# Performance work log

Measured on AMD Instinct MI355X. Metric: run time of the kernel, lower is better.

Reference implementation:

```python
import jax, jax.numpy as jnp
import numpy as np

T, A, E, N, W, HID, FD = 4096, 1024, 512, 32768, 10, 150, 20
GI = 2 * A + E  # 2560
BINS = jnp.array([1, 2, 3, 4, 8, 16, 32, 64], dtype=jnp.int32)


def _mlp(x, W1, b1, W2, b2, W3, b3):
    # Score module: Linear->ReLU->Linear->ReLU->Linear->1 (dropout is a no-op in eval)
    h = jax.nn.relu(x @ W1 + b1)
    h = jax.nn.relu(h @ W2 + b2)
    return h @ W3 + b3


def setup_inputs() -> dict:
    key = jax.random.key(0)
    ks = jax.random.split(key, 20)
    s = 0.02
    inp = {
        "states": jax.random.normal(ks[0], (T, A), jnp.float32),
        "embeds": jax.random.normal(ks[1], (T, E), jnp.float32),
        "span_starts": jax.random.randint(ks[2], (N,), 0, T - W, jnp.int32),
        "span_widths": jax.random.randint(ks[3], (N,), 1, W + 1, jnp.int32),
        # attention Score params (input A)
        "Wa1": jax.random.normal(ks[4], (A, HID)) * s, "ba1": jnp.zeros((HID,)),
        "Wa2": jax.random.normal(ks[5], (HID, HID)) * s, "ba2": jnp.zeros((HID,)),
        "Wa3": jax.random.normal(ks[6], (HID, 1)) * s, "ba3": jnp.zeros((1,)),
        # width Feature embedding table: len(bins)+1 = 9 rows
        "width_emb": jax.random.normal(ks[7], (9, FD)) * s,
        # mention Score params (input GI + FD)
        "Ws1": jax.random.normal(ks[8], (GI + FD, HID)) * s, "bs1": jnp.zeros((HID,)),
        "Ws2": jax.random.normal(ks[9], (HID, HID)) * s, "bs2": jnp.zeros((HID,)),
        "Ws3": jax.random.normal(ks[10], (HID, 1)) * s, "bs3": jnp.zeros((1,)),
    }
    return inp


def reference(states, embeds, span_starts, span_widths,
              Wa1, ba1, Wa2, ba2, Wa3, ba3, width_emb,
              Ws1, bs1, Ws2, bs2, Ws3, bs3):
    # per-token attention logits  [T]
    attns = _mlp(states, Wa1, ba1, Wa2, ba2, Wa3, ba3).squeeze(-1)
    offs = jnp.arange(W)                                   # [W]
    pos = span_starts[:, None] + offs[None, :]             # [N, W]
    mask = offs[None, :] < span_widths[:, None]            # ragged span mask
    pos_c = jnp.clip(pos, 0, T - 1)
    logit = jnp.where(mask, attns[pos_c], -jnp.inf)        # [N, W]
    w = jax.nn.softmax(logit, axis=1)                      # per-span softmax
    attn_sum = jnp.einsum('nw,nwe->ne', w, embeds[pos_c])  # [N, E]
    ends = span_starts + span_widths - 1
    bin_idx = jnp.sum(span_widths[:, None] >= BINS[None, :], axis=1)
    size = width_emb[bin_idx]                              # [N, FD]
    g = jnp.concatenate([states[span_starts], states[ends], attn_sum, size], axis=1)
    scores = _mlp(g, Ws1, bs1, Ws2, bs2, Ws3, bs3).squeeze(-1)  # [N]
    return scores
```

## Files before the change

### kernel.cpp

```cpp
#include <hip/hip_runtime.h>
#include <math.h>

#define T_TOK 4096
#define A_DIM 1024
#define E_DIM 512
#define N_SPAN 32768
#define W_MAX 10
#define HID 150
#define FD 20

#define PR  160
#define KP2 160

#define WS_ATTNS 0
#define WS_PB    4096
#define WS_WPACK 1314816
#define WS_SB    1627856
#define WS_EB    3725008
#define PB_P0 0
#define PB_P1 655360
#define PB_P2 1310720
#define PB_P3 1966080
#define WP_ST  0
#define WP_V   491520
#define WP_A2  573440
#define WP_S2  599040
#define WP_WE1 624640
#define WP_TOTAL 626080
#define SB_PIECES 524288
#define EB_PIECES 262144
#define PK_ITEMS (WP_TOTAL + SB_PIECES + EB_PIECES)

typedef short  bf16x8 __attribute__((ext_vector_type(8)));
typedef float  f32x4  __attribute__((ext_vector_type(4)));

__device__ __forceinline__ float4 ld4(const float* p) { return *(const float4*)p; }

__device__ __forceinline__ unsigned short f2bf(float f) {
    unsigned u = __float_as_uint(f);
    unsigned r = u + 0x7fffu + ((u >> 16) & 1u);
    return (unsigned short)(r >> 16);
}
__device__ __forceinline__ float bf2f(short s) {
    return __uint_as_float(((unsigned)(unsigned short)s) << 16);
}
__device__ __forceinline__ bf16x8 cvt_frag(const float* p) {
    float4 u = ld4(p), v = ld4(p + 4);
    bf16x8 f;
    f[0] = (short)f2bf(u.x); f[1] = (short)f2bf(u.y);
    f[2] = (short)f2bf(u.z); f[3] = (short)f2bf(u.w);
    f[4] = (short)f2bf(v.x); f[5] = (short)f2bf(v.y);
    f[6] = (short)f2bf(v.z); f[7] = (short)f2bf(v.w);
    return f;
}

__global__ __launch_bounds__(256) void prepack_kernel(
    const float* __restrict__ states, const float* __restrict__ embeds,
    const float* __restrict__ Wa1, const float* __restrict__ Ws1,
    const float* __restrict__ Wa2, const float* __restrict__ Ws2,
    const float* __restrict__ width_emb,
    unsigned short* __restrict__ wp, unsigned short* __restrict__ Sb,
    unsigned short* __restrict__ Eb)
{
    int idx = blockIdx.x * 256 + threadIdx.x;
    if (idx >= PK_ITEMS) return;
    if (idx < WP_TOTAL) {
        float v = 0.f;
        if (idx < WP_V) {
            int gidx = idx / 163840, r = idx % 163840;
            int ngrp = r / 81920, r2 = r % 81920;
            int c = r2 / 2560, d = r2 % 2560;
            int n = d >> 5, qsw = (d >> 3) & 3, off = d & 7;
            int q = qsw ^ ((n >> 1) & 3);
            int k = c * 32 + q * 8 + off;
            int gn = ngrp * 80 + n;
            const float* W = (gidx == 0) ? Wa1 : Ws1 + (size_t)(gidx - 1) * 1024 * HID;
            if (gn < HID) v = W[(size_t)k * HID + gn];
        } else if (idx < WP_A2) {
            int r = idx - WP_V;
            int ngrp = r / 40960, r2 = r % 40960;
            int c = r2 / 2560, d = r2 % 2560;
            int n = d >> 5, qsw = (d >> 3) & 3, off = d & 7;
            int q = qsw ^ ((n >> 1) & 3);
            int k = c * 32 + q * 8 + off;
            int gn = ngrp * 80 + n;
            if (gn < HID) v = Ws1[(size_t)(2048 + k) * HID + gn];
        } else if (idx < WP_S2) {
            int e = idx - WP_A2;
            int n = e / KP2, k = e % KP2;
            if (n < HID && k < HID) v = Wa2[(size_t)k * HID + n];
        } else if (idx < WP_WE1) {
            int e = idx - WP_S2;
            int n = e / KP2, k = e % KP2;
            if (n < HID && k < HID) v = Ws2[(size_t)k * HID + n];
        } else {
            int e = idx - WP_WE1;
            int b = e / KP2, n = e % KP2;
            if (n < HID)
                for (int k = 0; k < FD; ++k)
                    v = fmaf(width_emb[b * FD + k], Ws1[(size_t)(2560 + k) * HID + n], v);
        }
        wp[idx] = f2bf(v);
    } else if (idx < WP_TOTAL + SB_PIECES) {
        int p = idx - WP_TOTAL;
        int mb = p >> 11, r = p & 2047;
        int c = r >> 6, d8 = r & 63;
        int m = d8 >> 2, qsw = d8 & 3;
        int q = qsw ^ ((m >> 1) & 3);
        const float* src = states + (size_t)(mb * 16 + m) * A_DIM + c * 32 + q * 8;
        *(bf16x8*)(Sb + (size_t)p * 8) = cvt_frag(src);
    } else {
        int p = idx - WP_TOTAL - SB_PIECES;
        int mb = p >> 10, r = p & 1023;
        int c = r >> 6, d8 = r & 63;
        int m = d8 >> 2, qsw = d8 & 3;
        int q = qsw ^ ((m >> 1) & 3);
        const float* src = embeds + (size_t)(mb * 16 + m) * E_DIM + c * 32 + q * 8;
        *(bf16x8*)(Eb + (size_t)p * 8) = cvt_frag(src);
    }
}

template<int NCH>
__device__ __forceinline__ void gemm_reg(
    const unsigned short* __restrict__ pA0, const unsigned short* __restrict__ pA1,
    const unsigned short* __restrict__ pB, f32x4 (&acc)[2][5])
{
    bf16x8 a0[2], a1[2], bb[2][5];
#define LDC(c, s) { \
        a0[s] = *(const bf16x8*)(pA0 + (size_t)(c) * 512); \
        a1[s] = *(const bf16x8*)(pA1 + (size_t)(c) * 512); \
        _Pragma("unroll") \
        for (int t = 0; t < 5; ++t) \
            bb[s][t] = *(const bf16x8*)(pB + (size_t)(c) * 2560 + t * 512); }
    LDC(0, 0);
#pragma unroll
    for (int c = 0; c < NCH; ++c) {
        const int s = c & 1;
        if (c + 1 < NCH) LDC(c + 1, s ^ 1);
#pragma unroll
        for (int t = 0; t < 5; ++t) {
            acc[0][t] = __builtin_amdgcn_mfma_f32_16x16x32_bf16(a0[s], bb[s][t], acc[0][t], 0, 0, 0);
            acc[1][t] = __builtin_amdgcn_mfma_f32_16x16x32_bf16(a1[s], bb[s][t], acc[1][t], 0, 0, 0);
        }
    }
#undef LDC
}

__global__ __launch_bounds__(128) void token_kernel(
    const unsigned short* __restrict__ Sb, const unsigned short* __restrict__ Eb,
    const unsigned short* __restrict__ wp, unsigned short* __restrict__ Pb,
    const float* __restrict__ ba1, const float* __restrict__ ba2,
    const float* __restrict__ Wa3, const float* __restrict__ ba3,
    float* __restrict__ attns)
{
    __shared__ __align__(16) unsigned short sHb[32][168];

    const int wv = threadIdx.x >> 6;
    const int lane = threadIdx.x & 63, l15 = lane & 15, quad = lane >> 4;
    const int bl = l15 * 32 + ((quad ^ ((l15 >> 1) & 3)) * 8);
    const int b = blockIdx.x;
    const int ngrp = wv;

    f32x4 acc[2][5];
#pragma unroll
    for (int mt = 0; mt < 2; ++mt)
#pragma unroll
        for (int t = 0; t < 5; ++t)
#pragma unroll
            for (int i = 0; i < 4; ++i) acc[mt][t][i] = 0.f;

    int mb32, gidx;
    if (b < 384) {
        const int t = b * 2 + wv;
        mb32 = t / 6;
        gidx = (t % 6) >> 1;
        const unsigned short* pA0 = Sb + (size_t)(mb32 * 2) * 16384 + bl;
        const unsigned short* pA1 = pA0 + 16384;
        const unsigned short* pB  = wp + WP_ST + gidx * 163840 + ngrp * 81920 + bl;
        gemm_reg<32>(pA0, pA1, pB, acc);
    } else {
        mb32 = b - 384;
        gidx = 3;
        const unsigned short* pA0 = Eb + (size_t)(mb32 * 2) * 8192 + bl;
        const unsigned short* pA1 = pA0 + 8192;
        const unsigned short* pB  = wp + WP_V + ngrp * 40960 + bl;
        gemm_reg<16>(pA0, pA1, pB, acc);
    }

    if (gidx == 0) {
#pragma unroll
        for (int mt = 0; mt < 2; ++mt)
#pragma unroll
            for (int t = 0; t < 5; ++t) {
                const int col = ngrp * 80 + t * 16 + l15;
                const float b1 = (col < HID) ? ba1[col] : 0.f;
#pragma unroll
                for (int i = 0; i < 4; ++i)
                    sHb[mt * 16 + quad * 4 + i][col] =
                        (col < HID) ? f2bf(fmaxf(acc[mt][t][i] + b1, 0.f))
                                    : (unsigned short)0;
            }
        __syncthreads();
        const int t0 = mb32 * 32 + wv * 16;
        f32x4 a2[10];
#pragma unroll
        for (int nt = 0; nt < 10; ++nt)
#pragma unroll
            for (int i = 0; i < 4; ++i) a2[nt][i] = 0.f;

        const unsigned short* prow = &sHb[wv * 16 + l15][0];
        const unsigned short* bb = wp + WP_A2 + l15 * KP2 + quad * 8;
#pragma unroll
        for (int c = 0; c < 5; ++c) {
            const int k0 = c * 32;
            bf16x8 af = *(const bf16x8*)(prow + k0 + quad * 8);
#pragma unroll
            for (int nt = 0; nt < 10; ++nt) {
                bf16x8 bf = *(const bf16x8*)(bb + nt * 16 * KP2 + k0);
                a2[nt] = __builtin_amdgcn_mfma_f32_16x16x32_bf16(af, bf, a2[nt], 0, 0, 0);
            }
        }
        float sc[4] = {0.f, 0.f, 0.f, 0.f};
#pragma unroll
        for (int nt = 0; nt < 10; ++nt) {
            const int col = nt * 16 + l15;
            const float w3 = (col < HID) ? Wa3[col] : 0.f;
            const float b2 = (col < HID) ? ba2[col] : 0.f;
#pragma unroll
            for (int i = 0; i < 4; ++i)
                sc[i] = fmaf(fmaxf(a2[nt][i] + b2, 0.f), w3, sc[i]);
        }
#pragma unroll
        for (int off = 8; off >= 1; off >>= 1)
#pragma unroll
            for (int i = 0; i < 4; ++i) sc[i] += __shfl_down(sc[i], off, 16);
        if (l15 == 0) {
            const float b3 = ba3[0];
#pragma unroll
            for (int i = 0; i < 4; ++i) attns[t0 + quad * 4 + i] = sc[i] + b3;
        }
    } else {
        unsigned short* Pg = Pb + (size_t)gidx * 655360;
#pragma unroll
        for (int mt = 0; mt < 2; ++mt)
#pragma unroll
            for (int t = 0; t < 5; ++t) {
                const int col = ngrp * 80 + t * 16 + l15;
#pragma unroll
                for (int i = 0; i < 4; ++i)
                    Pg[(size_t)(mb32 * 32 + mt * 16 + quad * 4 + i) * PR + col] =
                        (col < HID) ? f2bf(acc[mt][t][i]) : (unsigned short)0;
            }
    }
}

__global__ __launch_bounds__(256) void span_kernel(
    const unsigned short* __restrict__ Pb, const float* __restrict__ attns,
    const unsigned short* __restrict__ wp,
    const int* __restrict__ span_starts, const int* __restrict__ span_widths,
    const float* __restrict__ bs1, const float* __restrict__ bs2,
    const float* __restrict__ Ws3, const float* __restrict__ bs3,
    float* __restrict__ out)
{
    __shared__ unsigned short sHb[32][168];
    __shared__ float s_wgt[32][W_MAX];
    __shared__ int s_st[32], s_wd[32], s_bin[32], s_oid[32], s_wdr[32];
    __shared__ float sPart[4][32];
    __shared__ float sb1[KP2];

    const int tid = threadIdx.x;
    const int n0s = blockIdx.x * 32;

    if (tid < KP2) sb1[tid] = (tid < HID) ? bs1[tid] : 0.f;
    int st = 0, wd = 0;
    if (tid < 32) {
        st = span_starts[n0s + tid];
        wd = span_widths[n0s + tid];
        s_wdr[tid] = wd;
    }
    __syncthreads();
    if (tid < 32) {
        int rank = 0;
#pragma unroll
        for (int j = 0; j < 32; ++j) {
            const int wj = s_wdr[j];
            rank += (wj < wd) || (wj == wd && j < tid);
        }
        s_st[rank] = st; s_wd[rank] = wd; s_oid[rank] = tid;
        s_bin[rank] = (wd >= 1) + (wd >= 2) + (wd >= 3) + (wd >= 4) +
                      (wd >= 8) + (wd >= 16) + (wd >= 32) + (wd >= 64);
        float lg[W_MAX];
        float m = -1e30f;
#pragma unroll
        for (int w = 0; w < W_MAX; ++w)
            if (w < wd) { float a = attns[st + w]; lg[w] = a; m = fmaxf(m, a); }
        float sum = 0.f;
#pragma unroll
        for (int w = 0; w < W_MAX; ++w) {
            float e = (w < wd) ? __expf(lg[w] - m) : 0.f;
            lg[w] = e; sum += e;
        }
        float inv = 1.f / sum;
#pragma unroll
        for (int w = 0; w < W_MAX; ++w) s_wgt[rank][w] = lg[w] * inv;
    }
    __syncthreads();

    {
        const unsigned short* P1b = Pb + PB_P1;
        const unsigned short* P2b = Pb + PB_P2;
        const unsigned short* P3b = Pb + PB_P3;
        const unsigned short* WEb = wp + WP_WE1;
        const int s = tid >> 3, jl = tid & 7;
        const int sst = s_st[s], swd = s_wd[s];
        const size_t rs = (size_t)sst * PR;
        const size_t re = (size_t)(sst + swd - 1) * PR;
        const size_t rb = (size_t)s_bin[s] * PR;
        for (int c = jl; c < 20; c += 8) {
            const int j = c * 8;
            bf16x8 u1 = *(const bf16x8*)(P1b + rs + j);
            bf16x8 u2 = *(const bf16x8*)(P2b + re + j);
            bf16x8 uw = *(const bf16x8*)(WEb + rb + j);
            float acc[8];
#pragma unroll
            for (int i = 0; i < 8; ++i)
                acc[i] = bf2f(u1[i]) + bf2f(u2[i]) + bf2f(uw[i]) + sb1[j + i];
#pragma unroll
            for (int w = 0; w < W_MAX; ++w) {
                if (w < swd) {
                    float wt = s_wgt[s][w];
                    bf16x8 uv = *(const bf16x8*)(P3b + rs + (size_t)w * PR + j);
#pragma unroll
                    for (int i = 0; i < 8; ++i)
                        acc[i] = fmaf(wt, bf2f(uv[i]), acc[i]);
                }
            }
            bf16x8 pk;
#pragma unroll
            for (int i = 0; i < 8; ++i) pk[i] = (short)f2bf(fmaxf(acc[i], 0.f));
            *(bf16x8*)&sHb[s][j] = pk;
        }
    }
    __syncthreads();

    const int wv = tid >> 6, lane = tid & 63, l15 = lane & 15, quad = lane >> 4;
    const int nb = (wv < 2) ? wv * 3 : 6 + (wv - 2) * 2;
    const int cnt = (wv < 2) ? 3 : 2;

    f32x4 a2[2][3];
#pragma unroll
    for (int mt = 0; mt < 2; ++mt)
#pragma unroll
        for (int t = 0; t < 3; ++t)
#pragma unroll
            for (int i = 0; i < 4; ++i) a2[mt][t][i] = 0.f;

#pragma unroll
    for (int c = 0; c < 5; ++c) {
        int k0 = c * 32;
        bf16x8 af0 = *(const bf16x8*)&sHb[l15][k0 + quad * 8];
        bf16x8 af1 = *(const bf16x8*)&sHb[16 + l15][k0 + quad * 8];
#pragma unroll
        for (int t = 0; t < 3; ++t) {
            if (t < cnt) {
                bf16x8 b = *(const bf16x8*)(wp + WP_S2 +
                            (size_t)((nb + t) * 16 + l15) * KP2 + k0 + quad * 8);
                a2[0][t] = __builtin_amdgcn_mfma_f32_16x16x32_bf16(af0, b, a2[0][t], 0, 0, 0);
                a2[1][t] = __builtin_amdgcn_mfma_f32_16x16x32_bf16(af1, b, a2[1][t], 0, 0, 0);
            }
        }
    }

    float sc[2][4];
#pragma unroll
    for (int mt = 0; mt < 2; ++mt)
#pragma unroll
        for (int i = 0; i < 4; ++i) sc[mt][i] = 0.f;
#pragma unroll
    for (int t = 0; t < 3; ++t) {
        if (t < cnt) {
            int col = (nb + t) * 16 + l15;
            float w3 = (col < HID) ? Ws3[col] : 0.f;
            float b2 = (col < HID) ? bs2[col] : 0.f;
#pragma unroll
            for (int mt = 0; mt < 2; ++mt)
#pragma unroll
                for (int i = 0; i < 4; ++i)
                    sc[mt][i] = fmaf(fmaxf(a2[mt][t][i] + b2, 0.f), w3, sc[mt][i]);
        }
    }
#pragma unroll
    for (int off = 8; off >= 1; off >>= 1)
#pragma unroll
        for (int mt = 0; mt < 2; ++mt)
#pragma unroll
            for (int i = 0; i < 4; ++i)
                sc[mt][i] += __shfl_down(sc[mt][i], off, 16);
    if (l15 == 0) {
#pragma unroll
        for (int mt = 0; mt < 2; ++mt)
#pragma unroll
            for (int i = 0; i < 4; ++i)
                sPart[wv][mt * 16 + quad * 4 + i] = sc[mt][i];
    }
    __syncthreads();
    if (tid < 32)
        out[n0s + s_oid[tid]] = sPart[0][tid] + sPart[1][tid] + sPart[2][tid] +
                                sPart[3][tid] + bs3[0];
}

extern "C" void kernel_launch(void* const* d_in, const int* in_sizes, int n_in,
                              void* d_out, int out_size, void* d_ws, size_t ws_size,
                              hipStream_t stream)
{
    const float* states      = (const float*)d_in[0];
    const float* embeds      = (const float*)d_in[1];
    const int*   span_starts = (const int*)d_in[2];
    const int*   span_widths = (const int*)d_in[3];
    const float* Wa1 = (const float*)d_in[4];
    const float* ba1 = (const float*)d_in[5];
    const float* Wa2 = (const float*)d_in[6];
    const float* ba2 = (const float*)d_in[7];
    const float* Wa3 = (const float*)d_in[8];
    const float* ba3 = (const float*)d_in[9];
    const float* width_emb = (const float*)d_in[10];
    const float* Ws1 = (const float*)d_in[11];
    const float* bs1 = (const float*)d_in[12];
    const float* Ws2 = (const float*)d_in[13];
    const float* bs2 = (const float*)d_in[14];
    const float* Ws3 = (const float*)d_in[15];
    const float* bs3 = (const float*)d_in[16];
    float* out = (float*)d_out;

    float* ws    = (float*)d_ws;
    float* attns = ws + WS_ATTNS;
    unsigned short* Pb    = (unsigned short*)(ws + WS_PB);
    unsigned short* wpack = (unsigned short*)(ws + WS_WPACK);
    unsigned short* Sb    = (unsigned short*)(ws + WS_SB);
    unsigned short* Eb    = (unsigned short*)(ws + WS_EB);

    hipLaunchKernelGGL(prepack_kernel, dim3((PK_ITEMS + 255) / 256), dim3(256), 0, stream,
                       states, embeds, Wa1, Ws1, Wa2, Ws2, width_emb,
                       wpack, Sb, Eb);
    hipLaunchKernelGGL(token_kernel, dim3(512), dim3(128), 0, stream,
                       Sb, Eb, wpack, Pb, ba1, ba2, Wa3, ba3, attns);
    hipLaunchKernelGGL(span_kernel, dim3(N_SPAN / 32), dim3(256), 0, stream,
                       Pb, attns, wpack, span_starts, span_widths,
                       bs1, bs2, Ws3, bs3, out);
}
```

Baseline: 153.7 us.

## Stream token GEMM operands into LDS via async global_load_lds pipeline

The token kernel's GEMM now stages A and B fragments through LDS using direct global-to-LDS DMA loads, with a 3-deep ring for B and double buffering for A, gated by vmcnt waits, in place of register double-buffered global loads. Block-to-tile mapping is also reordered so consecutive blocks share the same weight group across 8 M-tiles, which is meant to improve L2 reuse of weights. The LDS buffer is reused for the hidden-layer tile after a barrier. This adds LDS traffic and depends on correct manual vmcnt counts, which would break if the compiler reorders or inserts memory ops.

```diff
diff --git a/kernel.cpp b/kernel.cpp
--- a/kernel.cpp
+++ b/kernel.cpp
@@ -52,6 +52,15 @@
     f[4] = (short)f2bf(v.x); f[5] = (short)f2bf(v.y);
     f[6] = (short)f2bf(v.z); f[7] = (short)f2bf(v.w);
     return f;
+}
+
+typedef const __attribute__((address_space(1))) unsigned int as1_u32;
+typedef __attribute__((address_space(3))) unsigned int as3_u32;
+__device__ __forceinline__ void dma16(const void* g, void* l) {
+    __builtin_amdgcn_global_load_lds((as1_u32*)g, (as3_u32*)l, 16, 0, 0);
+}
+template<int N> __device__ __forceinline__ void waitv() {
+    asm volatile("s_waitcnt vmcnt(%0)" :: "n"(N) : "memory");
 }
 
 __global__ __launch_bounds__(256) void prepack_kernel(
@@ -120,30 +129,39 @@
     }
 }
 
-template<int NCH>
-__device__ __forceinline__ void gemm_reg(
-    const unsigned short* __restrict__ pA0, const unsigned short* __restrict__ pA1,
-    const unsigned short* __restrict__ pB, f32x4 (&acc)[2][5])
+template<int NC, int ATILE>
+__device__ __forceinline__ void gemm_dma32(
+    const unsigned short* __restrict__ srcA, const unsigned short* __restrict__ srcB,
+    unsigned short (*__restrict__ bufB)[2560], unsigned short (*__restrict__ bufA)[1024],
+    int lane, int bl, f32x4 (&acc)[2][5])
 {
-    bf16x8 a0[2], a1[2], bb[2][5];
-#define LDC(c, s) { \
-        a0[s] = *(const bf16x8*)(pA0 + (size_t)(c) * 512); \
-        a1[s] = *(const bf16x8*)(pA1 + (size_t)(c) * 512); \
-        _Pragma("unroll") \
-        for (int t = 0; t < 5; ++t) \
-            bb[s][t] = *(const bf16x8*)(pB + (size_t)(c) * 2560 + t * 512); }
-    LDC(0, 0);
-#pragma unroll
-    for (int c = 0; c < NCH; ++c) {
-        const int s = c & 1;
-        if (c + 1 < NCH) LDC(c + 1, s ^ 1);
+#define DMB(c) { _Pragma("unroll")                                           \
+        for (int i = 0; i < 5; ++i)                                          \
+            dma16(srcB + (size_t)(c) * 2560 + i * 512 + lane * 8,            \
+                  &bufB[(c) % 3][i * 512]); }
+#define DMA_(c) {                                                            \
+        dma16(srcA + (size_t)(c) * 512 + lane * 8, &bufA[(c) & 1][0]);       \
+        dma16(srcA + ATILE + (size_t)(c) * 512 + lane * 8, &bufA[(c) & 1][512]); }
+    DMB(0); DMA_(0); DMB(1);
+#pragma unroll
+    for (int c = 0; c < NC; ++c) {
+        if (c + 1 < NC) DMA_(c + 1);
+        if (c + 2 < NC) DMB(c + 2);
+        if (c + 2 < NC)      waitv<12>();
+        else if (c + 1 < NC) waitv<7>();
+        else                 waitv<0>();
+        bf16x8 af0 = *(const bf16x8*)(&bufA[c & 1][0]   + bl);
+        bf16x8 af1 = *(const bf16x8*)(&bufA[c & 1][512] + bl);
+        const unsigned short* bb = &bufB[c % 3][0];
 #pragma unroll
         for (int t = 0; t < 5; ++t) {
-            acc[0][t] = __builtin_amdgcn_mfma_f32_16x16x32_bf16(a0[s], bb[s][t], acc[0][t], 0, 0, 0);
-            acc[1][t] = __builtin_amdgcn_mfma_f32_16x16x32_bf16(a1[s], bb[s][t], acc[1][t], 0, 0, 0);
-        }
-    }
-#undef LDC
+            bf16x8 bf = *(const bf16x8*)(bb + t * 512 + bl);
+            acc[0][t] = __builtin_amdgcn_mfma_f32_16x16x32_bf16(af0, bf, acc[0][t], 0, 0, 0);
+            acc[1][t] = __builtin_amdgcn_mfma_f32_16x16x32_bf16(af1, bf, acc[1][t], 0, 0, 0);
+        }
+    }
+#undef DMB
+#undef DMA_
 }
 
 __global__ __launch_bounds__(128) void token_kernel(
@@ -153,13 +171,13 @@
     const float* __restrict__ Wa3, const float* __restrict__ ba3,
     float* __restrict__ attns)
 {
-    __shared__ __align__(16) unsigned short sHb[32][168];
+    __shared__ __align__(16) unsigned short bufB[2][3][2560];
+    __shared__ __align__(16) unsigned short bufA[2][2][1024];
 
     const int wv = threadIdx.x >> 6;
     const int lane = threadIdx.x & 63, l15 = lane & 15, quad = lane >> 4;
     const int bl = l15 * 32 + ((quad ^ ((l15 >> 1) & 3)) * 8);
     const int b = blockIdx.x;
-    const int ngrp = wv;
 
     f32x4 acc[2][5];
 #pragma unroll
@@ -171,28 +189,29 @@
 
     int mb32, gidx;
     if (b < 384) {
-        const int t = b * 2 + wv;
-        mb32 = t / 6;
-        gidx = (t % 6) >> 1;
-        const unsigned short* pA0 = Sb + (size_t)(mb32 * 2) * 16384 + bl;
-        const unsigned short* pA1 = pA0 + 16384;
-        const unsigned short* pB  = wp + WP_ST + gidx * 163840 + ngrp * 81920 + bl;
-        gemm_reg<32>(pA0, pA1, pB, acc);
+        const int x = b & 7, r = b >> 3;
+        gidx = r % 3;
+        mb32 = (r / 3) * 8 + x;
+        const unsigned short* srcA = Sb + (size_t)mb32 * 32768;
+        const unsigned short* srcB = wp + WP_ST + gidx * 163840 + wv * 81920;
+        gemm_dma32<32, 16384>(srcA, srcB, bufB[wv], bufA[wv], lane, bl, acc);
     } else {
-        mb32 = b - 384;
+        const int e = b - 384;
+        mb32 = (e >> 3) * 8 + (e & 7);
         gidx = 3;
-        const unsigned short* pA0 = Eb + (size_t)(mb32 * 2) * 8192 + bl;
-        const unsigned short* pA1 = pA0 + 8192;
-        const unsigned short* pB  = wp + WP_V + ngrp * 40960 + bl;
-        gemm_reg<16>(pA0, pA1, pB, acc);
+        const unsigned short* srcA = Eb + (size_t)mb32 * 16384;
+        const unsigned short* srcB = wp + WP_V + wv * 40960;
+        gemm_dma32<16, 8192>(srcA, srcB, bufB[wv], bufA[wv], lane, bl, acc);
     }
 
     if (gidx == 0) {
+        unsigned short (*sHb)[168] = (unsigned short (*)[168])&bufB[0][0][0];
+        __syncthreads();
 #pragma unroll
         for (int mt = 0; mt < 2; ++mt)
 #pragma unroll
             for (int t = 0; t < 5; ++t) {
-                const int col = ngrp * 80 + t * 16 + l15;
+                const int col = wv * 80 + t * 16 + l15;
                 const float b1 = (col < HID) ? ba1[col] : 0.f;
 #pragma unroll
                 for (int i = 0; i < 4; ++i)
@@ -245,7 +264,7 @@
         for (int mt = 0; mt < 2; ++mt)
 #pragma unroll
             for (int t = 0; t < 5; ++t) {
-                const int col = ngrp * 80 + t * 16 + l15;
+                const int col = wv * 80 + t * 16 + l15;
 #pragma unroll
                 for (int i = 0; i < 4; ++i)
                     Pg[(size_t)(mb32 * 32 + mt * 16 + quad * 4 + i) * PR + col] =
```

After: 146.4 us. -4.7%, faster.
